# Kernel optimization log

Measured on AMD Instinct MI355X. Metric: run time of the kernel, lower is better.

Reference implementation:

```python
import jax, jax.numpy as jnp
import numpy as np

N = 50000        # nodes
E = 800000       # edges
H = 128          # hidden_channels
NH = 4           # num_heads
HD = H // NH     # head_dim
EPS = 1e-5       # LayerNorm eps (torch default)


def setup_inputs() -> dict:
    key = jax.random.key(0)
    ks = jax.random.split(key, 16)
    s = 0.02
    return {
        "x": jax.random.normal(ks[0], (N, H), dtype=jnp.float32),
        "edge_index": jax.random.randint(ks[1], (2, E), 0, N, dtype=jnp.int64),
        "Wq": jax.random.normal(ks[2], (H, H), dtype=jnp.float32) * s,
        "bq": jnp.zeros((H,), jnp.float32),
        "Wk": jax.random.normal(ks[3], (H, H), dtype=jnp.float32) * s,
        "bk": jnp.zeros((H,), jnp.float32),
        "Wv": jax.random.normal(ks[4], (H, H), dtype=jnp.float32) * s,
        "bv": jnp.zeros((H,), jnp.float32),
        "W1": jax.random.normal(ks[5], (2 * H, H), dtype=jnp.float32) * s,
        "b1": jnp.zeros((H,), jnp.float32),
        "ln_g": jnp.ones((H,), jnp.float32),
        "ln_b": jnp.zeros((H,), jnp.float32),
        "W2": jax.random.normal(ks[6], (H, H), dtype=jnp.float32) * s,
        "b2": jnp.zeros((H,), jnp.float32),
    }


def reference(x, edge_index, Wq, bq, Wk, bk, Wv, bv, W1, b1, ln_g, ln_b, W2, b2):
    n = x.shape[0]
    row, col = edge_index[0], edge_index[1]
    # dense projections, split heads: [N, NH, HD]
    Q = (x @ Wq + bq).reshape(n, NH, HD)
    K = (x @ Wk + bk).reshape(n, NH, HD)
    V = (x @ Wv + bv).reshape(n, NH, HD)
    # edge-wise gather + per-head dot product: [E, NH]
    scores = (Q[row] * K[col]).sum(-1) / jnp.sqrt(jnp.float32(HD))
    # segment softmax over edges grouped by destination node (row)
    m = jax.ops.segment_max(scores, row, num_segments=n)        # [N, NH]
    m = jnp.where(jnp.isfinite(m), m, 0.0)                      # empty segments -> 0
    e = jnp.exp(scores - m[row])                                # [E, NH]
    denom = jax.ops.segment_sum(e, row, num_segments=n)         # [N, NH]
    w = e / denom[row]                                          # [E, NH]
    # weighted scatter-add aggregation: [N, H]
    msg = (w[..., None] * V[col]).reshape(-1, NH * HD)          # [E, H]
    agg = jax.ops.segment_sum(msg, row, num_segments=n)         # [N, H]
    # MLP: Linear -> ReLU -> LayerNorm -> Linear, plus residual
    h = jax.nn.relu(jnp.concatenate([x, agg], axis=-1) @ W1 + b1)
    mu = h.mean(-1, keepdims=True)
    var = ((h - mu) ** 2).mean(-1, keepdims=True)
    h = (h - mu) / jnp.sqrt(var + EPS) * ln_g + ln_b
    return h @ W2 + b2 + x
```

## Files before the change

kernel.cpp:

```cpp
#include <hip/hip_runtime.h>
#include <hip/hip_bf16.h>

#define NN 50000
#define HH 128
#define NHEAD 4
#define HD 32
#define EE 800000
#define LN_EPS 1e-5f
#define ROWS_PAD 50048
#define SCAN_NB 98
#define QKV_NB 782

typedef __bf16 bf16x8 __attribute__((ext_vector_type(8)));
typedef short  s16x8  __attribute__((ext_vector_type(8)));
typedef float  f32x4  __attribute__((ext_vector_type(4)));
typedef _Float16 h2   __attribute__((ext_vector_type(2)));

__device__ __forceinline__ f32x4 mfma_bf16(s16x8 a, s16x8 b, f32x4 c) {
    return __builtin_amdgcn_mfma_f32_16x16x32_bf16((bf16x8)a, (bf16x8)b, c, 0, 0, 0);
}

__device__ __forceinline__ unsigned short f2bf(float f) {
    union { float f; unsigned int u; } v; v.f = f;
    unsigned int u = v.u + 0x7FFFu + ((v.u >> 16) & 1u);
    return (unsigned short)(u >> 16);
}
__device__ __forceinline__ float bf2f(unsigned short h) {
    union { unsigned int u; float f; } v; v.u = ((unsigned int)h) << 16;
    return v.f;
}
__device__ __forceinline__ float bflo(unsigned int w) { return __uint_as_float(w << 16); }
__device__ __forceinline__ float bfhi(unsigned int w) { return __uint_as_float(w & 0xffff0000u); }

__device__ __forceinline__ unsigned short f2h(float f) {
    _Float16 h = (_Float16)f;
    return __builtin_bit_cast(unsigned short, h);
}

#if defined(__has_builtin)
#if __has_builtin(__builtin_amdgcn_fdot2)
#define HAVE_FDOT2 1
#endif
#endif

__device__ __forceinline__ float fdot2u(unsigned int a, unsigned int b, float c) {
#ifdef HAVE_FDOT2
    return __builtin_amdgcn_fdot2(__builtin_bit_cast(h2, a), __builtin_bit_cast(h2, b), c, false);
#else
    h2 ha = __builtin_bit_cast(h2, a), hb = __builtin_bit_cast(h2, b);
    return c + (float)ha[0] * (float)hb[0] + (float)ha[1] * (float)hb[1];
#endif
}

__device__ __forceinline__ int probe_is64(const unsigned int* __restrict__ buf) {
    unsigned int acc = 0u;
    #pragma unroll
    for (int i = 0; i < 64; ++i) acc |= buf[2 * i + 1];
    return acc == 0u;
}

__global__ void pack_w_kernel(const float* __restrict__ Wq, const float* __restrict__ Wk,
                              const float* __restrict__ Wv, const float* __restrict__ W1,
                              const float* __restrict__ W2, unsigned short* __restrict__ wf,
                              int* __restrict__ deg) {
    int i = blockIdx.x * blockDim.x + threadIdx.x;
    if (i < NN) deg[i] = 0;
    if (i >= 98304) return;
    float val;
    if (i < 49152) {
        int j = i & 7, lane = (i >> 3) & 63, kk = (i >> 9) & 3, nt = i >> 11;
        int k = kk * 32 + (lane >> 4) * 8 + j;
        int n = nt * 16 + (lane & 15);
        const float* W = (n < 128) ? Wq : ((n < 256) ? Wk : Wv);
        val = W[k * HH + (n & 127)];
    } else if (i < 81920) {
        int local = i - 49152;
        int j = local & 7, lane = (local >> 3) & 63, kk = (local >> 9) & 7, nt = local >> 12;
        int k = kk * 32 + (lane >> 4) * 8 + j;
        int n = nt * 16 + (lane & 15);
        val = W1[k * HH + n];
    } else {
        int local = i - 81920;
        int j = local & 7, lane = (local >> 3) & 63, kk = (local >> 9) & 3, nt = local >> 11;
        int k = kk * 32 + (lane >> 4) * 8 + j;
        int n = nt * 16 + (lane & 15);
        val = W2[k * HH + n];
    }
    wf[i] = f2bf(val);
}

__global__ void hist_kernel(const void* __restrict__ ei,
                            int* __restrict__ deg, int* __restrict__ rank) {
    const int is64 = probe_is64((const unsigned int*)ei);
    int i = (blockIdx.x * blockDim.x + threadIdx.x) * 2;
    if (i >= EE) return;
    int r0, r1;
    if (is64) {
        longlong2 rv = *(const longlong2*)((const long long*)ei + i);
        r0 = (int)rv.x; r1 = (int)rv.y;
    } else {
        int2 rv = *(const int2*)((const int*)ei + i);
        r0 = rv.x; r1 = rv.y;
    }
    int ra = atomicAdd(&deg[r0], 1);
    int rb = atomicAdd(&deg[r1], 1);
    *(int2*)(rank + i) = make_int2(ra, rb);
}

__global__ __launch_bounds__(256) void scan_qkvx_kernel(
        const int* __restrict__ deg, int* __restrict__ rstart,
        const float* __restrict__ x, const unsigned short* __restrict__ wf,
        const float* __restrict__ bq, const float* __restrict__ bk, const float* __restrict__ bv,
        unsigned short* __restrict__ xa,
        unsigned short* __restrict__ Qb, unsigned short* __restrict__ Kb,
        unsigned short* __restrict__ Vb) {
    const int b = blockIdx.x;
    const int lane = threadIdx.x & 63;
    const int wave = threadIdx.x >> 6;

    if (b < SCAN_NB) {
        __shared__ int red[4];
        __shared__ int wsum[4];
        const int t = threadIdx.x;
        const int base = b * 512;
        int pre = 0;
        for (int k = t; k < base; k += 256) pre += deg[k];
        #pragma unroll
        for (int o = 1; o < 64; o <<= 1) pre += __shfl_xor(pre, o);
        if (lane == 0) red[wave] = pre;
        const int i0 = base + 2 * t, i1 = i0 + 1;
        int d0 = (i0 < NN) ? deg[i0] : 0;
        int d1 = (i1 < NN) ? deg[i1] : 0;
        int ps = d0 + d1;
        int incl = ps;
        #pragma unroll
        for (int o = 1; o < 64; o <<= 1) {
            int u = __shfl_up(incl, o);
            if (lane >= o) incl += u;
        }
        if (lane == 63) wsum[wave] = incl;
        __syncthreads();
        const int boff = red[0] + red[1] + red[2] + red[3];
        int woff = 0;
        for (int k = 0; k < wave; ++k) woff += wsum[k];
        const int excl = boff + woff + incl - ps;
        if (i0 < NN) rstart[i0] = excl;
        if (i1 < NN) rstart[i1] = excl + d0;
        if (b == 0 && t == 0) rstart[NN] = EE;
        return;
    }

    const int row0 = (b - SCAN_NB) * 64 + wave * 16;
    const int arow = row0 + (lane & 15);
    const int kbase = (lane >> 4) * 8;

    s16x8 a[4];
    if (arow < NN) {
        const float* xp = x + (size_t)arow * HH + kbase;
        #pragma unroll
        for (int kk = 0; kk < 4; ++kk) {
            float4 f0 = *(const float4*)(xp + kk * 32);
            float4 f1 = *(const float4*)(xp + kk * 32 + 4);
            s16x8 av;
            av[0] = (short)f2bf(f0.x); av[1] = (short)f2bf(f0.y);
            av[2] = (short)f2bf(f0.z); av[3] = (short)f2bf(f0.w);
            av[4] = (short)f2bf(f1.x); av[5] = (short)f2bf(f1.y);
            av[6] = (short)f2bf(f1.z); av[7] = (short)f2bf(f1.w);
            a[kk] = av;
            *(s16x8*)(xa + (size_t)arow * 256 + kbase + kk * 32) = av;
        }
    } else {
        #pragma unroll
        for (int kk = 0; kk < 4; ++kk) a[kk] = (s16x8)0;
    }

    f32x4 acc[24];
    #pragma unroll
    for (int nt = 0; nt < 24; ++nt) acc[nt] = (f32x4){0.f, 0.f, 0.f, 0.f};

    const s16x8* wfv = (const s16x8*)wf;
    #pragma unroll
    for (int nt = 0; nt < 24; ++nt) {
        #pragma unroll
        for (int kk = 0; kk < 4; ++kk) {
            s16x8 bb = wfv[(nt * 4 + kk) * 64 + lane];
            acc[nt] = mfma_bf16(a[kk], bb, acc[nt]);
        }
    }

    const int colb = lane & 15;
    const int rbase = row0 + (lane >> 4) * 4;
    #pragma unroll
    for (int nt = 0; nt < 24; ++nt) {
        const int mtx = nt >> 3;
        const int nc = (nt & 7) * 16 + colb;
        const float* bias_p = (mtx == 0) ? bq : ((mtx == 1) ? bk : bv);
        unsigned short* O = (mtx == 0) ? Qb : ((mtx == 1) ? Kb : Vb);
        float bias = bias_p[nc];
        #pragma unroll
        for (int r = 0; r < 4; ++r) {
            float v = acc[nt][r] + bias;
            O[(size_t)(rbase + r) * 128 + nc] = (mtx == 2) ? f2bf(v) : f2h(v);
        }
    }
}

__global__ void scatter_kernel(const void* __restrict__ ei,
                               const int* __restrict__ rank, const int* __restrict__ rstart,
                               int* __restrict__ colS) {
    const int is64 = probe_is64((const unsigned int*)ei);
    int i = (blockIdx.x * blockDim.x + threadIdx.x) * 2;
    if (i >= EE) return;
    int r0, r1, c0, c1;
    if (is64) {
        longlong2 rv = *(const longlong2*)((const long long*)ei + i);
        longlong2 cv = *(const longlong2*)((const long long*)ei + EE + i);
        r0 = (int)rv.x; r1 = (int)rv.y;
        c0 = (int)cv.x; c1 = (int)cv.y;
    } else {
        int2 rv = *(const int2*)((const int*)ei + i);
        int2 cv = *(const int2*)((const int*)ei + EE + i);
        r0 = rv.x; r1 = rv.y;
        c0 = cv.x; c1 = cv.y;
    }
    int2 rk = *(const int2*)(rank + i);
    colS[rstart[r0] + rk.x] = c0;
    colS[rstart[r1] + rk.y] = c1;
}

__global__ __launch_bounds__(256) void attn_kernel(
        const unsigned short* __restrict__ Qb, const unsigned short* __restrict__ Kb,
        const unsigned short* __restrict__ Vb, const int* __restrict__ rstart,
        const int* __restrict__ colS, unsigned short* __restrict__ xa) {
    const int wave = threadIdx.x >> 6;
    const int lane = threadIdx.x & 63;
    const int i = blockIdx.x * 4 + wave;
    if (i >= NN) return;
    const int h = lane & 3;
    const int le = lane >> 2;
    const int half = lane >> 5;
    const int sl = lane & 31;
    const int g2 = sl >> 3;
    const int e0 = rstart[i], e1 = rstart[i + 1];
    const int deg = e1 - e0;

    uint4 q[4];
    {
        const uint4* qp = (const uint4*)(Qb + (size_t)i * 128 + h * 32);
        #pragma unroll
        for (int c = 0; c < 4; ++c) q[c] = qp[c];
    }

    float l = 0.f;
    float acc0 = 0.f, acc1 = 0.f, acc2 = 0.f, acc3 = 0.f;

    for (int c0 = 0; c0 < deg; c0 += 16) {
        const int cnt = min(16, deg - c0);
        int col = 0;
        if (le < cnt) col = colS[e0 + c0 + le];
        const uint4* kp = (const uint4*)(Kb + (size_t)col * 128 + h * 32);
        uint4 k0 = kp[0], k1 = kp[1], k2 = kp[2], k3 = kp[3];
        float d0 = 0.f, d1 = 0.f, d2 = 0.f, d3 = 0.f;
        d0 = fdot2u(k0.x, q[0].x, d0); d0 = fdot2u(k0.y, q[0].y, d0);
        d0 = fdot2u(k0.z, q[0].z, d0); d0 = fdot2u(k0.w, q[0].w, d0);
        d1 = fdot2u(k1.x, q[1].x, d1); d1 = fdot2u(k1.y, q[1].y, d1);
        d1 = fdot2u(k1.z, q[1].z, d1); d1 = fdot2u(k1.w, q[1].w, d1);
        d2 = fdot2u(k2.x, q[2].x, d2); d2 = fdot2u(k2.y, q[2].y, d2);
        d2 = fdot2u(k2.z, q[2].z, d2); d2 = fdot2u(k2.w, q[2].w, d2);
        d3 = fdot2u(k3.x, q[3].x, d3); d3 = fdot2u(k3.y, q[3].y, d3);
        d3 = fdot2u(k3.z, q[3].z, d3); d3 = fdot2u(k3.w, q[3].w, d3);
        const float s = ((d0 + d1) + (d2 + d3)) * 0.17677669529663689f;
        const float p = (le < cnt) ? __expf(s) : 0.f;
        float ps = p;
        ps += __shfl_xor(ps, 4);
        ps += __shfl_xor(ps, 8);
        ps += __shfl_xor(ps, 16);
        ps += __shfl_xor(ps, 32);
        l += ps;
        #pragma unroll
        for (int e2 = 0; e2 < 8; ++e2) {
            const int e = 2 * e2 + half;
            const int   cbc = __shfl(col, 4 * e);
            const float pbc = __shfl(p, 4 * e + g2);
            const uint2 v2 = *(const uint2*)(Vb + (size_t)cbc * 128 + 4 * sl);
            acc0 += pbc * bflo(v2.x);
            acc1 += pbc * bfhi(v2.x);
            acc2 += pbc * bflo(v2.y);
            acc3 += pbc * bfhi(v2.y);
        }
    }

    acc0 += __shfl_xor(acc0, 32);
    acc1 += __shfl_xor(acc1, 32);
    acc2 += __shfl_xor(acc2, 32);
    acc3 += __shfl_xor(acc3, 32);
    const float lf = __shfl(l, g2);
    const float rinv = (lf > 0.f) ? 1.f / lf : 0.f;
    if (half == 0) {
        uint2 o;
        o.x = ((unsigned int)f2bf(acc1 * rinv) << 16) | (unsigned int)f2bf(acc0 * rinv);
        o.y = ((unsigned int)f2bf(acc3 * rinv) << 16) | (unsigned int)f2bf(acc2 * rinv);
        *(uint2*)(xa + (size_t)i * 256 + 128 + 4 * sl) = o;
    }
}

#define HROW 136
__global__ __launch_bounds__(256) void mlp_fused_kernel(
        const unsigned short* __restrict__ xa, const unsigned short* __restrict__ w1f,
        const float* __restrict__ b1, const float* __restrict__ ln_g,
        const float* __restrict__ ln_b, const unsigned short* __restrict__ w2f,
        const float* __restrict__ b2, float* __restrict__ out) {
    __shared__ unsigned short hs[64 * HROW];
    const int wave = threadIdx.x >> 6, lane = threadIdx.x & 63;
    const int row0 = blockIdx.x * 64 + wave * 16;
    const int arow = row0 + (lane & 15);
    const int colb = lane & 15;

    s16x8 a[8];
    const unsigned short* ap = xa + (size_t)arow * 256 + (lane >> 4) * 8;
    #pragma unroll
    for (int kk = 0; kk < 8; ++kk) a[kk] = *(const s16x8*)(ap + kk * 32);

    f32x4 acc[8];
    #pragma unroll
    for (int nt = 0; nt < 8; ++nt) acc[nt] = (f32x4){0.f, 0.f, 0.f, 0.f};

    const s16x8* w1v = (const s16x8*)w1f;
    #pragma unroll
    for (int nt = 0; nt < 8; ++nt) {
        #pragma unroll
        for (int kk = 0; kk < 8; ++kk) {
            s16x8 b = w1v[(nt * 8 + kk) * 64 + lane];
            acc[nt] = mfma_bf16(a[kk], b, acc[nt]);
        }
    }

    #pragma unroll
    for (int nt = 0; nt < 8; ++nt) {
        float bias = b1[nt * 16 + colb];
        #pragma unroll
        for (int r = 0; r < 4; ++r) {
            float v = acc[nt][r] + bias;
            acc[nt][r] = v > 0.f ? v : 0.f;
        }
    }
    float mu[4], rs[4];
    #pragma unroll
    for (int r = 0; r < 4; ++r) {
        float s = 0.f, q = 0.f;
        #pragma unroll
        for (int nt = 0; nt < 8; ++nt) { float v = acc[nt][r]; s += v; q += v * v; }
        #pragma unroll
        for (int msk = 1; msk < 16; msk <<= 1) {
            s += __shfl_xor(s, msk, 16);
            q += __shfl_xor(q, msk, 16);
        }
        float m_ = s * (1.f / 128.f);
        float var = q * (1.f / 128.f) - m_ * m_;
        mu[r] = m_;
        rs[r] = rsqrtf(var + LN_EPS);
    }
    const int lrbase = wave * 16 + (lane >> 4) * 4;
    #pragma unroll
    for (int nt = 0; nt < 8; ++nt) {
        int col = nt * 16 + colb;
        float g = ln_g[col], bb = ln_b[col];
        #pragma unroll
        for (int r = 0; r < 4; ++r) {
            float hv = (acc[nt][r] - mu[r]) * rs[r] * g + bb;
            hs[(lrbase + r) * HROW + col] = f2bf(hv);
        }
    }
    __syncthreads();

    const int la = wave * 16 + (lane & 15);
    s16x8 a2[4];
    const unsigned short* hp = hs + la * HROW + (lane >> 4) * 8;
    #pragma unroll
    for (int kk = 0; kk < 4; ++kk) a2[kk] = *(const s16x8*)(hp + kk * 32);

    f32x4 acc2[8];
    #pragma unroll
    for (int nt = 0; nt < 8; ++nt) acc2[nt] = (f32x4){0.f, 0.f, 0.f, 0.f};

    const s16x8* w2v = (const s16x8*)w2f;
    #pragma unroll
    for (int nt = 0; nt < 8; ++nt) {
        #pragma unroll
        for (int kk = 0; kk < 4; ++kk) {
            s16x8 b = w2v[(nt * 4 + kk) * 64 + lane];
            acc2[nt] = mfma_bf16(a2[kk], b, acc2[nt]);
        }
    }

    const int rbase = row0 + (lane >> 4) * 4;
    #pragma unroll
    for (int nt = 0; nt < 8; ++nt) {
        int col = nt * 16 + colb;
        float bias = b2[col];
        #pragma unroll
        for (int r = 0; r < 4; ++r) {
            int row = rbase + r;
            if (row < NN)
                out[(size_t)row * 128 + col] =
                    acc2[nt][r] + bias + bf2f(xa[(size_t)row * 256 + col]);
        }
    }
}

extern "C" void kernel_launch(void* const* d_in, const int* in_sizes, int n_in,
                              void* d_out, int out_size, void* d_ws, size_t ws_size,
                              hipStream_t stream) {
    const float* x    = (const float*)d_in[0];
    const void*  ei   = d_in[1];
    const float* Wq   = (const float*)d_in[2];
    const float* bq   = (const float*)d_in[3];
    const float* Wk   = (const float*)d_in[4];
    const float* bk   = (const float*)d_in[5];
    const float* Wv   = (const float*)d_in[6];
    const float* bv   = (const float*)d_in[7];
    const float* W1   = (const float*)d_in[8];
    const float* b1   = (const float*)d_in[9];
    const float* ln_g = (const float*)d_in[10];
    const float* ln_b = (const float*)d_in[11];
    const float* W2   = (const float*)d_in[12];
    const float* b2   = (const float*)d_in[13];
    float* out = (float*)d_out;

    char* ws = (char*)d_ws;
    size_t off = 0;
    auto alloc = [&](size_t bytes) {
        size_t o = off;
        off = (off + bytes + 255) & ~(size_t)255;
        return o;
    };
    size_t deg_o  = alloc((size_t)NN * sizeof(int));
    size_t rank_o = alloc((size_t)EE * sizeof(int));
    size_t rs_o   = alloc((size_t)(NN + 1) * sizeof(int));
    size_t colS_o = alloc((size_t)EE * sizeof(int));
    size_t xa_o   = alloc((size_t)ROWS_PAD * 256 * sizeof(unsigned short));
    size_t wf_o   = alloc((size_t)98304 * sizeof(unsigned short));
    size_t Qb_o   = alloc((size_t)ROWS_PAD * 128 * sizeof(unsigned short));
    size_t Kb_o   = alloc((size_t)ROWS_PAD * 128 * sizeof(unsigned short));
    size_t Vb_o   = alloc((size_t)ROWS_PAD * 128 * sizeof(unsigned short));

    int* deg             = (int*)(ws + deg_o);
    int* rank            = (int*)(ws + rank_o);
    int* rstart          = (int*)(ws + rs_o);
    int* colS            = (int*)(ws + colS_o);
    unsigned short* xa   = (unsigned short*)(ws + xa_o);
    unsigned short* wf   = (unsigned short*)(ws + wf_o);
    unsigned short* Qb   = (unsigned short*)(ws + Qb_o);
    unsigned short* Kb   = (unsigned short*)(ws + Kb_o);
    unsigned short* Vb   = (unsigned short*)(ws + Vb_o);

    pack_w_kernel<<<98304 / 256, 256, 0, stream>>>(Wq, Wk, Wv, W1, W2, wf, deg);
    hist_kernel<<<(EE / 2 + 255) / 256, 256, 0, stream>>>(ei, deg, rank);
    scan_qkvx_kernel<<<SCAN_NB + QKV_NB, 256, 0, stream>>>(
        deg, rstart, x, wf, bq, bk, bv, xa, Qb, Kb, Vb);
    scatter_kernel<<<(EE / 2 + 255) / 256, 256, 0, stream>>>(ei, rank, rstart, colS);
    attn_kernel<<<(NN + 3) / 4, 256, 0, stream>>>(Qb, Kb, Vb, rstart, colS, xa);
    mlp_fused_kernel<<<ROWS_PAD / 64, 256, 0, stream>>>(
        xa, wf + 49152, b1, ln_g, ln_b, wf + 81920, b2, out);
}
```

Before: 188.1 us.

## Process four edges per thread in CSR build and two chunks per attention step

The histogram and scatter kernels now handle four edges per thread with wider vector loads, which halves the thread count. The attention loop processes two 16-edge chunks per iteration so more K and V gathers are in flight at once, with a single-chunk tail afterwards. The MLP residual now reads the fp32 x directly instead of the bf16 copy in xa, which also changes numerics slightly. The costs are higher register pressure in attention and less parallelism in the CSR kernels.

```diff
diff --git a/kernel.cpp b/kernel.cpp
--- a/kernel.cpp
+++ b/kernel.cpp
@@ -50,6 +50,21 @@
     h2 ha = __builtin_bit_cast(h2, a), hb = __builtin_bit_cast(h2, b);
     return c + (float)ha[0] * (float)hb[0] + (float)ha[1] * (float)hb[1];
 #endif
+}
+
+__device__ __forceinline__ float dot32(const uint4 k0, const uint4 k1,
+                                       const uint4 k2, const uint4 k3,
+                                       const uint4 q[4]) {
+    float d0 = 0.f, d1 = 0.f, d2 = 0.f, d3 = 0.f;
+    d0 = fdot2u(k0.x, q[0].x, d0); d0 = fdot2u(k0.y, q[0].y, d0);
+    d0 = fdot2u(k0.z, q[0].z, d0); d0 = fdot2u(k0.w, q[0].w, d0);
+    d1 = fdot2u(k1.x, q[1].x, d1); d1 = fdot2u(k1.y, q[1].y, d1);
+    d1 = fdot2u(k1.z, q[1].z, d1); d1 = fdot2u(k1.w, q[1].w, d1);
+    d2 = fdot2u(k2.x, q[2].x, d2); d2 = fdot2u(k2.y, q[2].y, d2);
+    d2 = fdot2u(k2.z, q[2].z, d2); d2 = fdot2u(k2.w, q[2].w, d2);
+    d3 = fdot2u(k3.x, q[3].x, d3); d3 = fdot2u(k3.y, q[3].y, d3);
+    d3 = fdot2u(k3.z, q[3].z, d3); d3 = fdot2u(k3.w, q[3].w, d3);
+    return (d0 + d1) + (d2 + d3);
 }
 
 __device__ __forceinline__ int probe_is64(const unsigned int* __restrict__ buf) {
@@ -92,19 +107,23 @@
 __global__ void hist_kernel(const void* __restrict__ ei,
                             int* __restrict__ deg, int* __restrict__ rank) {
     const int is64 = probe_is64((const unsigned int*)ei);
-    int i = (blockIdx.x * blockDim.x + threadIdx.x) * 2;
+    int i = (blockIdx.x * blockDim.x + threadIdx.x) * 4;
     if (i >= EE) return;
-    int r0, r1;
+    int r[4];
     if (is64) {
-        longlong2 rv = *(const longlong2*)((const long long*)ei + i);
-        r0 = (int)rv.x; r1 = (int)rv.y;
+        longlong2 a = *(const longlong2*)((const long long*)ei + i);
+        longlong2 b = *(const longlong2*)((const long long*)ei + i + 2);
+        r[0] = (int)a.x; r[1] = (int)a.y; r[2] = (int)b.x; r[3] = (int)b.y;
     } else {
-        int2 rv = *(const int2*)((const int*)ei + i);
-        r0 = rv.x; r1 = rv.y;
-    }
-    int ra = atomicAdd(&deg[r0], 1);
-    int rb = atomicAdd(&deg[r1], 1);
-    *(int2*)(rank + i) = make_int2(ra, rb);
+        int4 a = *(const int4*)((const int*)ei + i);
+        r[0] = a.x; r[1] = a.y; r[2] = a.z; r[3] = a.w;
+    }
+    int4 rk;
+    rk.x = atomicAdd(&deg[r[0]], 1);
+    rk.y = atomicAdd(&deg[r[1]], 1);
+    rk.z = atomicAdd(&deg[r[2]], 1);
+    rk.w = atomicAdd(&deg[r[3]], 1);
+    *(int4*)(rank + i) = rk;
 }
 
 __global__ __launch_bounds__(256) void scan_qkvx_kernel(
@@ -209,23 +228,27 @@
                                const int* __restrict__ rank, const int* __restrict__ rstart,
                                int* __restrict__ colS) {
     const int is64 = probe_is64((const unsigned int*)ei);
-    int i = (blockIdx.x * blockDim.x + threadIdx.x) * 2;
+    int i = (blockIdx.x * blockDim.x + threadIdx.x) * 4;
     if (i >= EE) return;
-    int r0, r1, c0, c1;
+    int r[4], c[4];
     if (is64) {
-        longlong2 rv = *(const longlong2*)((const long long*)ei + i);
-        longlong2 cv = *(const longlong2*)((const long long*)ei + EE + i);
-        r0 = (int)rv.x; r1 = (int)rv.y;
-        c0 = (int)cv.x; c1 = (int)cv.y;
+        longlong2 a = *(const longlong2*)((const long long*)ei + i);
+        longlong2 b = *(const longlong2*)((const long long*)ei + i + 2);
+        longlong2 ca = *(const longlong2*)((const long long*)ei + EE + i);
+        longlong2 cb = *(const longlong2*)((const long long*)ei + EE + i + 2);
+        r[0] = (int)a.x; r[1] = (int)a.y; r[2] = (int)b.x; r[3] = (int)b.y;
+        c[0] = (int)ca.x; c[1] = (int)ca.y; c[2] = (int)cb.x; c[3] = (int)cb.y;
     } else {
-        int2 rv = *(const int2*)((const int*)ei + i);
-        int2 cv = *(const int2*)((const int*)ei + EE + i);
-        r0 = rv.x; r1 = rv.y;
-        c0 = cv.x; c1 = cv.y;
-    }
-    int2 rk = *(const int2*)(rank + i);
-    colS[rstart[r0] + rk.x] = c0;
-    colS[rstart[r1] + rk.y] = c1;
+        int4 a = *(const int4*)((const int*)ei + i);
+        int4 ca = *(const int4*)((const int*)ei + EE + i);
+        r[0] = a.x; r[1] = a.y; r[2] = a.z; r[3] = a.w;
+        c[0] = ca.x; c[1] = ca.y; c[2] = ca.z; c[3] = ca.w;
+    }
+    int4 rk = *(const int4*)(rank + i);
+    colS[rstart[r[0]] + rk.x] = c[0];
+    colS[rstart[r[1]] + rk.y] = c[1];
+    colS[rstart[r[2]] + rk.z] = c[2];
+    colS[rstart[r[3]] + rk.w] = c[3];
 }
 
 __global__ __launch_bounds__(256) void attn_kernel(
@@ -253,23 +276,58 @@
 
     float l = 0.f;
     float acc0 = 0.f, acc1 = 0.f, acc2 = 0.f, acc3 = 0.f;
-
-    for (int c0 = 0; c0 < deg; c0 += 16) {
-        const int cnt = min(16, deg - c0);
+    const float scale = 0.17677669529663689f;
+
+    int c0 = 0;
+    for (; c0 + 16 < deg; c0 += 32) {
+        const int cntB = min(16, deg - c0 - 16);
+        const int colA = colS[e0 + c0 + le];
+        int colB = 0;
+        if (le < cntB) colB = colS[e0 + c0 + 16 + le];
+        const uint4* kpA = (const uint4*)(Kb + (size_t)colA * 128 + h * 32);
+        const uint4* kpB = (const uint4*)(Kb + (size_t)colB * 128 + h * 32);
+        uint4 a0 = kpA[0], a1 = kpA[1], a2 = kpA[2], a3 = kpA[3];
+        uint4 b0 = kpB[0], b1 = kpB[1], b2 = kpB[2], b3 = kpB[3];
+        const float sA = dot32(a0, a1, a2, a3, q) * scale;
+        const float sB = dot32(b0, b1, b2, b3, q) * scale;
+        const float pA = __expf(sA);
+        const float pB = (le < cntB) ? __expf(sB) : 0.f;
+        float ps = pA + pB;
+        ps += __shfl_xor(ps, 4);
+        ps += __shfl_xor(ps, 8);
+        ps += __shfl_xor(ps, 16);
+        ps += __shfl_xor(ps, 32);
+        l += ps;
+        #pragma unroll
+        for (int e2 = 0; e2 < 8; ++e2) {
+            const int e = 2 * e2 + half;
+            const int   cbc = __shfl(colA, 4 * e);
+            const float pbc = __shfl(pA, 4 * e + g2);
+            const uint2 v2 = *(const uint2*)(Vb + (size_t)cbc * 128 + 4 * sl);
+            acc0 += pbc * bflo(v2.x);
+            acc1 += pbc * bfhi(v2.x);
+            acc2 += pbc * bflo(v2.y);
+            acc3 += pbc * bfhi(v2.y);
+        }
+        #pragma unroll
+        for (int e2 = 0; e2 < 8; ++e2) {
+            const int e = 2 * e2 + half;
+            const int   cbc = __shfl(colB, 4 * e);
+            const float pbc = __shfl(pB, 4 * e + g2);
+            const uint2 v2 = *(const uint2*)(Vb + (size_t)cbc * 128 + 4 * sl);
+            acc0 += pbc * bflo(v2.x);
+            acc1 += pbc * bfhi(v2.x);
+            acc2 += pbc * bflo(v2.y);
+            acc3 += pbc * bfhi(v2.y);
+        }
+    }
+    if (c0 < deg) {
+        const int cnt = deg - c0;
         int col = 0;
         if (le < cnt) col = colS[e0 + c0 + le];
         const uint4* kp = (const uint4*)(Kb + (size_t)col * 128 + h * 32);
         uint4 k0 = kp[0], k1 = kp[1], k2 = kp[2], k3 = kp[3];
-        float d0 = 0.f, d1 = 0.f, d2 = 0.f, d3 = 0.f;
-        d0 = fdot2u(k0.x, q[0].x, d0); d0 = fdot2u(k0.y, q[0].y, d0);
-        d0 = fdot2u(k0.z, q[0].z, d0); d0 = fdot2u(k0.w, q[0].w, d0);
-        d1 = fdot2u(k1.x, q[1].x, d1); d1 = fdot2u(k1.y, q[1].y, d1);
-        d1 = fdot2u(k1.z, q[1].z, d1); d1 = fdot2u(k1.w, q[1].w, d1);
-        d2 = fdot2u(k2.x, q[2].x, d2); d2 = fdot2u(k2.y, q[2].y, d2);
-        d2 = fdot2u(k2.z, q[2].z, d2); d2 = fdot2u(k2.w, q[2].w, d2);
-        d3 = fdot2u(k3.x, q[3].x, d3); d3 = fdot2u(k3.y, q[3].y, d3);
-        d3 = fdot2u(k3.z, q[3].z, d3); d3 = fdot2u(k3.w, q[3].w, d3);
-        const float s = ((d0 + d1) + (d2 + d3)) * 0.17677669529663689f;
+        const float s = dot32(k0, k1, k2, k3, q) * scale;
         const float p = (le < cnt) ? __expf(s) : 0.f;
         float ps = p;
         ps += __shfl_xor(ps, 4);
@@ -309,7 +367,8 @@
         const unsigned short* __restrict__ xa, const unsigned short* __restrict__ w1f,
         const float* __restrict__ b1, const float* __restrict__ ln_g,
         const float* __restrict__ ln_b, const unsigned short* __restrict__ w2f,
-        const float* __restrict__ b2, float* __restrict__ out) {
+        const float* __restrict__ b2, const float* __restrict__ x,
+        float* __restrict__ out) {
     __shared__ unsigned short hs[64 * HROW];
     const int wave = threadIdx.x >> 6, lane = threadIdx.x & 63;
     const int row0 = blockIdx.x * 64 + wave * 16;
@@ -403,7 +462,7 @@
             int row = rbase + r;
             if (row < NN)
                 out[(size_t)row * 128 + col] =
-                    acc2[nt][r] + bias + bf2f(xa[(size_t)row * 256 + col]);
+                    acc2[nt][r] + bias + x[(size_t)row * 128 + col];
         }
     }
 }
@@ -455,11 +514,11 @@
     unsigned short* Vb   = (unsigned short*)(ws + Vb_o);
 
     pack_w_kernel<<<98304 / 256, 256, 0, stream>>>(Wq, Wk, Wv, W1, W2, wf, deg);
-    hist_kernel<<<(EE / 2 + 255) / 256, 256, 0, stream>>>(ei, deg, rank);
+    hist_kernel<<<(EE / 4 + 255) / 256, 256, 0, stream>>>(ei, deg, rank);
     scan_qkvx_kernel<<<SCAN_NB + QKV_NB, 256, 0, stream>>>(
         deg, rstart, x, wf, bq, bk, bv, xa, Qb, Kb, Vb);
-    scatter_kernel<<<(EE / 2 + 255) / 256, 256, 0, stream>>>(ei, rank, rstart, colS);
+    scatter_kernel<<<(EE / 4 + 255) / 256, 256, 0, stream>>>(ei, rank, rstart, colS);
     attn_kernel<<<(NN + 3) / 4, 256, 0, stream>>>(Qb, Kb, Vb, rstart, colS, xa);
     mlp_fused_kernel<<<ROWS_PAD / 64, 256, 0, stream>>>(
-        xa, wf + 49152, b1, ln_g, ln_b, wf + 81920, b2, out);
-}
+        xa, wf + 49152, b1, ln_g, ln_b, wf + 81920, b2, x, out);
+}
```

Result: slower. 195.3 us (+3.8%).
